# Kernel optimization log

Measured on AMD Instinct MI355X. Metric: run time of the kernel, lower is better.

The kernel has to match this reference:

```python
import jax, jax.numpy as jnp
import numpy as np

IN_C = 256
GROUPS = 32
ED = 256  # ResnetBlock embed_dim
EPS = 1e-5
B, L = 16, 2048


def setup_inputs() -> dict:
    key = jax.random.key(0)
    ks = jax.random.split(key, 8)

    def rn(k, shape, s=0.05):
        return jax.random.normal(k, shape, dtype=jnp.float32) * s

    d = {
        "x": jax.random.normal(ks[0], (B, IN_C, L), dtype=jnp.float32),
        "t": jax.random.normal(ks[1], (B, 256, 1), dtype=jnp.float32),
    }
    i = 2
    for p in ["r1", "r2"]:
        d[f"{p}_gn1_w"] = jnp.ones((IN_C,), jnp.float32)
        d[f"{p}_gn1_b"] = jnp.zeros((IN_C,), jnp.float32)
        d[f"{p}_c1_w"] = rn(ks[i], (ED, IN_C, 3)); i += 1
        d[f"{p}_c1_b"] = jnp.zeros((ED,), jnp.float32)
        d[f"{p}_gn2_w"] = jnp.ones((ED,), jnp.float32)
        d[f"{p}_gn2_b"] = jnp.zeros((ED,), jnp.float32)
        d[f"{p}_c2_w"] = rn(ks[i], (IN_C, ED, 3)); i += 1
        d[f"{p}_c2_b"] = jnp.zeros((IN_C,), jnp.float32)
    d["lin_w"] = rn(ks[i], (3 * IN_C, IN_C, 1))
    d["lin_b"] = jnp.zeros((3 * IN_C,), jnp.float32)
    return d


def _gn(x, w, b):
    # GroupNorm over (C//G, L) per group, affine per-channel
    Bx, C, Lx = x.shape
    xr = x.reshape(Bx, GROUPS, -1)
    m = xr.mean(-1, keepdims=True)
    v = xr.var(-1, keepdims=True)
    xr = (xr - m) * jax.lax.rsqrt(v + EPS)
    return xr.reshape(Bx, C, Lx) * w[None, :, None] + b[None, :, None]


def _conv(x, w, b, pad):
    y = jax.lax.conv_general_dilated(
        x, w, window_strides=(1,), padding=[(pad, pad)],
        dimension_numbers=("NCH", "OIH", "NCH"))
    return y + b[None, :, None]


def _res(x, t, gn1w, gn1b, c1w, c1b, gn2w, gn2b, c2w, c2b):
    h = _conv(jax.nn.relu(_gn(x, gn1w, gn1b)), c1w, c1b, 1) + t
    h = _conv(jax.nn.relu(_gn(h, gn2w, gn2b)), c2w, c2b, 1)
    return x + h


def reference(x, t,
              r1_gn1_w, r1_gn1_b, r1_c1_w, r1_c1_b, r1_gn2_w, r1_gn2_b, r1_c2_w, r1_c2_b,
              r2_gn1_w, r2_gn1_b, r2_c1_w, r2_c1_b, r2_gn2_w, r2_gn2_b, r2_c2_w, r2_c2_b,
              lin_w, lin_b):
    x = _res(x, t, r1_gn1_w, r1_gn1_b, r1_c1_w, r1_c1_b, r1_gn2_w, r1_gn2_b, r1_c2_w, r1_c2_b)
    kqv = _conv(x, lin_w, lin_b, 0)                      # (B, 3C, L)
    kt, qt, vt = jnp.split(kqv, 3, axis=1)               # each (B, C, L)
    scale = 1.0 / np.sqrt(x.shape[1]).astype(np.float32)
    scores = jnp.einsum("bcq,bck->bqk", qt, kt) * scale  # (B, L, L)
    attn = jax.nn.softmax(scores, axis=2)
    av = jnp.einsum("bqk,bck->bcq", attn, vt)            # (B, C, L)
    return _res(av, t, r2_gn1_w, r2_gn1_b, r2_c1_w, r2_c1_b, r2_gn2_w, r2_gn2_b, r2_c2_w, r2_c2_b)
```

## Files before the change

kernel.cpp:

```cpp
#include <hip/hip_runtime.h>

typedef unsigned short u16;
typedef unsigned int u32;
typedef __attribute__((ext_vector_type(8))) short bf16x8;
typedef __attribute__((ext_vector_type(4))) float f32x4;
typedef __attribute__((ext_vector_type(16))) float f32x16;

#define NB 16
#define NC 256
#define NL 2048
#define NG 32
#define EPS 1e-5f
#define QSC2 0.0901684401f
#define DEFER 11.54f
#define TROWS 2050
#define PHALF ((size_t)NB * NC * NL)

__device__ __forceinline__ float bf2f(u16 a) {
  union { unsigned u; float f; } v; v.u = (unsigned)a << 16; return v.f;
}
__device__ __forceinline__ u16 f2bf(float f) {
  union { float f; unsigned u; } v; v.f = f;
  return (u16)((v.u + 0x7fffu + ((v.u >> 16) & 1u)) >> 16);
}
__device__ __forceinline__ u32 cvtpk(float lo, float hi) {
  u32 r;
  asm("v_cvt_pk_bf16_f32 %0, %1, %2" : "=v"(r) : "v"(lo), "v"(hi));
  return r;
}
__device__ __forceinline__ float ex2(float x) {
  float r;
  asm("v_exp_f32 %0, %1" : "=v"(r) : "v"(x));
  return r;
}
__device__ __forceinline__ void gld16(const void* gsrc, void* ldst) {
  __builtin_amdgcn_global_load_lds(
      (const __attribute__((address_space(1))) void*)gsrc,
      (__attribute__((address_space(3))) void*)ldst, 16, 0, 0);
}

__global__ __launch_bounds__(256)
void pack_w(const float* __restrict__ w1, const float* __restrict__ w2,
            const float* __restrict__ w3, const float* __restrict__ w4,
            const float* __restrict__ lw, const float* __restrict__ lb,
            u16* __restrict__ Wp, u16* __restrict__ Wq, float* __restrict__ bq)
{
  const int a = blockIdx.y;
  const int gid = blockIdx.x * 256 + threadIdx.x;
  if (a < 4) {
    const float* w = a == 0 ? w1 : a == 1 ? w2 : a == 2 ? w3 : w4;
    const int d = gid >> 16, rem = gid & 65535;
    const int oc = rem >> 8, ic = rem & 255;
    Wp[a * 196608 + gid] = f2bf(w[(oc * 256 + ic) * 3 + d]);
  } else {
    const int oc = gid >> 8;
    const float s = (oc >= 256 && oc < 512) ? QSC2 : 1.0f;
    Wq[gid] = f2bf(lw[gid] * s);
    if (gid < 768) bq[gid] = lb[gid] * ((gid >= 256 && gid < 512) ? QSC2 : 1.0f);
  }
}

__global__ __launch_bounds__(256)
void stats_f32(const float* __restrict__ x, float2* __restrict__ pstat)
{
  const int blk = blockIdx.x;
  const float* p = x + (size_t)blk * NL + threadIdx.x * 8;
  const float4 a = ((const float4*)p)[0];
  const float4 c4 = ((const float4*)p)[1];
  float s = (a.x + a.y) + (a.z + a.w) + (c4.x + c4.y) + (c4.z + c4.w);
  float ss = a.x*a.x + a.y*a.y + a.z*a.z + a.w*a.w + c4.x*c4.x + c4.y*c4.y + c4.z*c4.z + c4.w*c4.w;
#pragma unroll
  for (int o = 32; o > 0; o >>= 1) { s += __shfl_down(s, o); ss += __shfl_down(ss, o); }
  __shared__ float2 red[4];
  if ((threadIdx.x & 63) == 0) red[threadIdx.x >> 6] = make_float2(s, ss);
  __syncthreads();
  if (threadIdx.x == 0)
    pstat[blk] = make_float2(red[0].x + red[1].x + red[2].x + red[3].x,
                             red[0].y + red[1].y + red[2].y + red[3].y);
}

__global__ __launch_bounds__(256)
void stats_T(const u16* __restrict__ inT, float2* __restrict__ pstat)
{
  const int chunk = blockIdx.x, b = blockIdx.y;
  const int t = threadIdx.x;
  const int c4 = (t & 63) * 4;
  float s[4] = {0.f, 0.f, 0.f, 0.f}, ss[4] = {0.f, 0.f, 0.f, 0.f};
  for (int j = 0; j < 32; ++j) {
    const int row = chunk * 128 + j * 4 + (t >> 6);
    const ushort4 h = *(const ushort4*)(inT + ((size_t)b * TROWS + 1 + row) * 256 + c4);
    const float v0 = bf2f(h.x), v1 = bf2f(h.y), v2 = bf2f(h.z), v3 = bf2f(h.w);
    s[0] += v0; ss[0] += v0 * v0;
    s[1] += v1; ss[1] += v1 * v1;
    s[2] += v2; ss[2] += v2 * v2;
    s[3] += v3; ss[3] += v3 * v3;
  }
  __shared__ float2 srs[256][4];
#pragma unroll
  for (int i = 0; i < 4; ++i) srs[t][i] = make_float2(s[i], ss[i]);
  __syncthreads();
  if (t < 64) {
#pragma unroll
    for (int r = 1; r < 4; ++r)
#pragma unroll
      for (int i = 0; i < 4; ++i) {
        s[i] += srs[t + 64 * r][i].x;
        ss[i] += srs[t + 64 * r][i].y;
      }
#pragma unroll
    for (int i = 0; i < 4; ++i)
      pstat[((size_t)b * 16 + chunk) * 256 + t * 4 + i] = make_float2(s[i], ss[i]);
  }
}

__global__ __launch_bounds__(256)
void apply_f32T(const float* __restrict__ x, const float2* __restrict__ pstat,
                const float* __restrict__ gw, const float* __restrict__ gb,
                u16* __restrict__ outT)
{
  __shared__ float2 chs[256];
  __shared__ float gm[32], gi[32];
  __shared__ float ta[256][33];
  const int t = threadIdx.x, b = blockIdx.y;
  const int L0 = blockIdx.x * 32;
  chs[t] = pstat[b * 256 + t];
  __syncthreads();
  if (t < 32) {
    float S = 0.f, SS = 0.f;
#pragma unroll
    for (int j = 0; j < 8; ++j) { S += chs[t * 8 + j].x; SS += chs[t * 8 + j].y; }
    const float mean = S * (1.f / 16384.f);
    const float var = SS * (1.f / 16384.f) - mean * mean;
    gm[t] = mean; gi[t] = rsqrtf(var + EPS);
  }
  const int cR = t >> 3, lq = (t & 7) * 4;
#pragma unroll
  for (int i = 0; i < 8; ++i) {
    const int c = i * 32 + cR;
    const float4 v = *(const float4*)&x[((size_t)b * NC + c) * NL + L0 + lq];
    ta[c][lq] = v.x; ta[c][lq + 1] = v.y; ta[c][lq + 2] = v.z; ta[c][lq + 3] = v.w;
  }
  __syncthreads();
  const int g = t & 31;
  float ga[8], be[8];
#pragma unroll
  for (int j = 0; j < 8; ++j) {
    ga[j] = gw[g * 8 + j] * gi[g];
    be[j] = gb[g * 8 + j] - gm[g] * ga[j];
  }
#pragma unroll
  for (int i = 0; i < 4; ++i) {
    const int chunk = i * 256 + t;
    const int row = chunk >> 5;
    const int ch8 = g * 8;
    u16 o[8];
#pragma unroll
    for (int j = 0; j < 8; ++j)
      o[j] = f2bf(fmaxf(fmaf(ta[ch8 + j][row], ga[j], be[j]), 0.f));
    *(bf16x8*)(outT + ((size_t)b * TROWS + 1 + L0 + row) * 256 + ch8) = *(bf16x8*)o;
  }
  if (blockIdx.x == 0 && t < 128) {
    const int r = (t >> 6) ? 2049 : 0;
    *(ushort4*)(outT + ((size_t)b * TROWS + r) * 256 + (t & 63) * 4) = (ushort4){0, 0, 0, 0};
  }
}

__global__ __launch_bounds__(256)
void apply_TT(const u16* __restrict__ inT, const float2* __restrict__ pstat,
              const float* __restrict__ gw, const float* __restrict__ gb,
              u16* __restrict__ outT)
{
  __shared__ float2 chs[256];
  __shared__ float gm[32], gi[32];
  const int t = threadIdx.x, b = blockIdx.y;
  {
    float S = 0.f, SS = 0.f;
#pragma unroll
    for (int p = 0; p < 16; ++p) {
      const float2 v = pstat[((size_t)b * 16 + p) * 256 + t];
      S += v.x; SS += v.y;
    }
    chs[t] = make_float2(S, SS);
  }
  __syncthreads();
  if (t < 32) {
    float S = 0.f, SS = 0.f;
#pragma unroll
    for (int j = 0; j < 8; ++j) { S += chs[t * 8 + j].x; SS += chs[t * 8 + j].y; }
    const float mean = S * (1.f / 16384.f);
    const float var = SS * (1.f / 16384.f) - mean * mean;
    gm[t] = mean; gi[t] = rsqrtf(var + EPS);
  }
  __syncthreads();
  const int g = t & 31;
  float ga[8], be[8];
#pragma unroll
  for (int j = 0; j < 8; ++j) {
    ga[j] = gw[g * 8 + j] * gi[g];
    be[j] = gb[g * 8 + j] - gm[g] * ga[j];
  }
#pragma unroll
  for (int j = 0; j < 16; ++j) {
    const int row = blockIdx.x * 128 + j * 8 + (t >> 5);
    const size_t off = ((size_t)b * TROWS + 1 + row) * 256 + g * 8;
    const bf16x8 h = *(const bf16x8*)(inT + off);
    u16 o[8];
#pragma unroll
    for (int i = 0; i < 8; ++i)
      o[i] = f2bf(fmaxf(fmaf(bf2f(((const u16*)&h)[i]), ga[i], be[i]), 0.f));
    *(bf16x8*)(outT + off) = *(bf16x8*)o;
  }
  if (blockIdx.x == 0 && t < 128) {
    const int r = (t >> 6) ? 2049 : 0;
    *(ushort4*)(outT + ((size_t)b * TROWS + r) * 256 + (t & 63) * 4) = (ushort4){0, 0, 0, 0};
  }
}

template<int OCT, int KD, bool HAS_T, int RESM>
__global__ __launch_bounds__(256, 2)
void conv_mfma(const u16* __restrict__ xT, const u16* __restrict__ Wp,
               const float* __restrict__ bias, const float* __restrict__ tadd,
               u16* __restrict__ outT, u16* __restrict__ vTout,
               const float* __restrict__ resf, float* __restrict__ outf)
{
  constexpr int DOFF = (KD == 3) ? 0 : 1;
  __shared__ __align__(16) u16 xs[2][130 * 128];
  const int lb = blockIdx.x * 128;
  const int ocb = blockIdx.y * 128;
  const int b = blockIdx.z;
  const int tid = threadIdx.x;
  const int w = tid >> 6, lane = tid & 63;
  const int l15 = lane & 15, lg = lane >> 4;
  const int woc = (w >> 1) * 64, wl = (w & 1) * 64;

  f32x4 acc[4][4];
#pragma unroll
  for (int i = 0; i < 4; ++i)
#pragma unroll
    for (int j = 0; j < 4; ++j) acc[i][j] = (f32x4){0.f, 0.f, 0.f, 0.f};

  const u16* xTb = xT + ((size_t)b * TROWS + lb) * 256;

  auto stageX = [&](int buf, int ich) {
    u16* xb = &xs[buf][0];
#pragma unroll
    for (int j = 0; j < 8; ++j) {
      const int slot = w * 512 + j * 64 + lane;
      const int row = slot >> 4, g0 = slot & 15;
      const int g = (g0 & 8) | ((g0 ^ row) & 7);
      gld16(xTb + (size_t)row * 256 + ich * 128 + g * 8, xb + (size_t)(w * 512 + j * 64) * 8);
    }
    if (w == 0 && lane < 32) {
      const int slot = 2048 + lane;
      const int row = slot >> 4, g0 = slot & 15;
      const int g = (g0 & 8) | ((g0 ^ row) & 7);
      gld16(xTb + (size_t)row * 256 + ich * 128 + g * 8, xb + (size_t)2048 * 8);
    }
  };
  auto loadW = [&](bf16x8 (&af)[KD][4], int p) {
    const int ich = p >> 2, kc = p & 3;
#pragma unroll
    for (int d = 0; d < KD; ++d)
#pragma unroll
      for (int mf = 0; mf < 4; ++mf)
        af[d][mf] = *(const bf16x8*)(Wp + ((size_t)d * OCT + ocb + woc + mf * 16 + l15) * 256
                                        + ich * 128 + kc * 32 + lg * 8);
  };

  bf16x8 afbuf[2][KD][4];
  stageX(0, 0);
  loadW(afbuf[0], 0);
  __syncthreads();
  stageX(1, 1);

#pragma unroll
  for (int p = 0; p < 8; ++p) {
    if (p == 4) __syncthreads();
    if (p < 7) loadW(afbuf[(p + 1) & 1], p + 1);
    const int kc = p & 3;
    const int gg = kc * 4 + lg;
    const char* xb = (const char*)&xs[p >> 2][0];
#pragma unroll
    for (int nf = 0; nf < 4; ++nf) {
#pragma unroll
      for (int d = 0; d < KD; ++d) {
        const int r = wl + nf * 16 + l15 + d + DOFF;
        const int gsr = (gg & 8) | ((gg ^ r) & 7);
        const bf16x8 bf = *(const bf16x8*)(xb + r * 256 + gsr * 16);
#pragma unroll
        for (int mf = 0; mf < 4; ++mf)
          acc[mf][nf] = __builtin_amdgcn_mfma_f32_16x16x32_bf16(afbuf[p & 1][d][mf], bf, acc[mf][nf], 0, 0, 0);
      }
    }
  }

  if (OCT == 768 && ocb >= 512) {
    __syncthreads();
    u16* tile = (u16*)&xs[0][0];
#pragma unroll
    for (int mf = 0; mf < 4; ++mf) {
      const int cl = woc + mf * 16 + lg * 4;
      const float4 bv = *(const float4*)&bias[ocb + cl];
#pragma unroll
      for (int nf = 0; nf < 4; ++nf) {
        const int ll = wl + nf * 16 + l15;
        const f32x4 a = acc[mf][nf];
        tile[(cl + 0) * 136 + ll] = f2bf(a[0] + bv.x);
        tile[(cl + 1) * 136 + ll] = f2bf(a[1] + bv.y);
        tile[(cl + 2) * 136 + ll] = f2bf(a[2] + bv.z);
        tile[(cl + 3) * 136 + ll] = f2bf(a[3] + bv.w);
      }
    }
    __syncthreads();
    const int cv0 = ocb - 512;
#pragma unroll
    for (int it = 0; it < 8; ++it) {
      const int chunk = it * 256 + tid;
      const int row = chunk >> 4, off = (chunk & 15) * 8;
      const bf16x8 v = *(const bf16x8*)&tile[row * 136 + off];
      *(bf16x8*)(vTout + ((size_t)b * NC + cv0 + row) * NL + lb + off) = v;
    }
    return;
  }

#pragma unroll
  for (int mf = 0; mf < 4; ++mf) {
    const int ocbase = ocb + woc + mf * 16 + lg * 4;
    float4 bv = *(const float4*)&bias[ocbase];
    if (HAS_T) {
      const float4 tv = *(const float4*)&tadd[b * 256 + ocbase];
      bv.x += tv.x; bv.y += tv.y; bv.z += tv.z; bv.w += tv.w;
    }
#pragma unroll
    for (int nf = 0; nf < 4; ++nf) {
      const int l = lb + wl + nf * 16 + l15;
      const f32x4 a = acc[mf][nf];
      float v0 = a[0] + bv.x, v1 = a[1] + bv.y, v2 = a[2] + bv.z, v3 = a[3] + bv.w;
      if (RESM >= 1) {
        const float* rp = resf + ((size_t)b * NC + ocbase) * NL + l;
        v0 += rp[0]; v1 += rp[NL]; v2 += rp[2 * (size_t)NL]; v3 += rp[3 * (size_t)NL];
      }
      if (RESM == 2) {
        float* op = outf + ((size_t)b * NC + ocbase) * NL + l;
        op[0] = v0; op[NL] = v1; op[2 * (size_t)NL] = v2; op[3 * (size_t)NL] = v3;
      } else if (OCT == 256) {
        ushort4 st = {f2bf(v0), f2bf(v1), f2bf(v2), f2bf(v3)};
        *(ushort4*)(outT + ((size_t)b * TROWS + 1 + l) * 256 + ocbase) = st;
      } else {
        ushort4 st = {f2bf(v0), f2bf(v1), f2bf(v2), f2bf(v3)};
        *(ushort4*)(outT + ((size_t)b * NL + l) * 512 + ocbase) = st;
      }
    }
  }
}

#define AKVB 32
#define ATILES 32

__global__ __launch_bounds__(256, 2)
void attn_mfma(const u16* __restrict__ kq, const u16* __restrict__ vT,
               u16* __restrict__ part, float2* __restrict__ stats)
{
  __shared__ u16 ks[2][32 * 256];
  __shared__ u16 vs[2][256 * 32];

  const int fid = blockIdx.x;
  const int xcd = fid & 7, idx = fid >> 3;
  const int b = (xcd << 1) | (idx & 1);
  const int rest = idx >> 1;
  const int qt = rest & 15, half = rest >> 4;
  const int kvbase = half * 1024;

  const int tid = threadIdx.x;
  const int w = tid >> 6, lane = tid & 63;
  const int l31 = lane & 31, lh = lane >> 5;
  const int q = qt * 128 + w * 32 + l31;

  const u16* kqb = kq + (size_t)b * NL * 512;
  const u16* vb  = vT + (size_t)b * NC * NL;

  auto stage = [&](int buf, int kv0) {
#pragma unroll
    for (int j = 0; j < 4; ++j) {
      const int slot = w * 256 + j * 64 + lane;
      const int r = slot >> 5, c = slot & 31;
      const int g = (c - r) & 31;
      gld16(kqb + (size_t)(kv0 + r) * 512 + g * 8, &ks[buf][(size_t)(w * 256 + j * 64) * 8]);
    }
#pragma unroll
    for (int j = 0; j < 4; ++j) {
      const int slot = w * 256 + j * 64 + lane;
      const int r = slot >> 2, c = slot & 3;
      const int g = (c - r - (r >> 2)) & 3;
      gld16(vb + (size_t)r * NL + kv0 + g * 8, &vs[buf][(size_t)(w * 256 + j * 64) * 8]);
    }
  };

  bf16x8 qf[16];
  {
    const u16* qp = kqb + (size_t)q * 512 + 256 + lh * 8;
#pragma unroll
    for (int kk = 0; kk < 16; ++kk) qf[kk] = *(const bf16x8*)(qp + kk * 16);
  }

  f32x16 o[8];
#pragma unroll
  for (int i = 0; i < 8; ++i)
    o[i] = (f32x16){0.f,0.f,0.f,0.f,0.f,0.f,0.f,0.f,0.f,0.f,0.f,0.f,0.f,0.f,0.f,0.f};
  float m = -1e30f, lsum = 0.f;

  stage(0, kvbase);
  __syncthreads();

  for (int t = 0; t < ATILES; ++t) {
    const int cur = t & 1;
    if (t + 1 < ATILES) stage(cur ^ 1, kvbase + (t + 1) * AKVB);
    const u16* kbase = &ks[cur][0];
    f32x16 s = (f32x16){0.f,0.f,0.f,0.f,0.f,0.f,0.f,0.f,0.f,0.f,0.f,0.f,0.f,0.f,0.f,0.f};
#pragma unroll
    for (int kk = 0; kk < 16; ++kk) {
      const int gn = 2 * kk + lh;
      const bf16x8 kf = *(const bf16x8*)(kbase + (l31 * 32 + ((gn + l31) & 31)) * 8);
      s = __builtin_amdgcn_mfma_f32_32x32x16_bf16(kf, qf[kk], s, 0, 0, 0);
    }
    float tm = s[0];
#pragma unroll
    for (int i = 1; i < 16; ++i) tm = fmaxf(tm, s[i]);
    tm = fmaxf(tm, __shfl_xor(tm, 32));
    if (!__all(tm <= m + DEFER)) {
      const float mn = fmaxf(m, tm);
      const float corr = ex2(m - mn);
      m = mn; lsum *= corr;
#pragma unroll
      for (int i = 0; i < 8; ++i) o[i] *= corr;
    }
    float sum = 0.f;
#pragma unroll
    for (int i = 0; i < 16; ++i) { s[i] = ex2(s[i] - m); sum += s[i]; }
    sum += __shfl_xor(sum, 32);
    lsum += sum;
    u32 pk[8];
#pragma unroll
    for (int i = 0; i < 8; ++i) pk[i] = cvtpk(s[2 * i], s[2 * i + 1]);
    const u16* vbase = &vs[cur][0];
#pragma unroll
    for (int ksx = 0; ksx < 2; ++ksx) {
      const int base = ksx * 4;
      const u32 send0 = lh ? pk[base + 0] : pk[base + 2];
      const u32 send1 = lh ? pk[base + 1] : pk[base + 3];
      const u32 r0 = (u32)__shfl_xor((int)send0, 32);
      const u32 r1 = (u32)__shfl_xor((int)send1, 32);
      union { u32 wd[4]; bf16x8 v; } pu;
      pu.wd[0] = lh ? r0 : pk[base + 0];
      pu.wd[1] = lh ? r1 : pk[base + 1];
      pu.wd[2] = lh ? pk[base + 2] : r0;
      pu.wd[3] = lh ? pk[base + 3] : r1;
      const bf16x8 pf = pu.v;
      const int gn = 2 * ksx + lh;
#pragma unroll
      for (int mf = 0; mf < 8; ++mf) {
        const int row = mf * 32 + l31;
        const bf16x8 vf = *(const bf16x8*)(vbase + (row * 4 + ((gn + row + (row >> 2)) & 3)) * 8);
        o[mf] = __builtin_amdgcn_mfma_f32_32x32x16_bf16(vf, pf, o[mf], 0, 0, 0);
      }
    }
    if (t + 1 < ATILES) __syncthreads();
  }
  u16* pp = part + half * PHALF + (size_t)b * NC * NL + q;
#pragma unroll
  for (int mf = 0; mf < 8; ++mf)
#pragma unroll
    for (int r = 0; r < 16; ++r) {
      const int c = mf * 32 + (r & 3) + 8 * (r >> 2) + 4 * lh;
      pp[(size_t)c * NL] = f2bf(o[mf][r]);
    }
  if (lane < 32)
    stats[((size_t)half * NB + b) * NL + q] = make_float2(m, lsum);
}

__global__ __launch_bounds__(256)
void attn_combine(const u16* __restrict__ part, const float2* __restrict__ stats,
                  float* __restrict__ av, float2* __restrict__ pstat)
{
  const int c = blockIdx.x, b = blockIdx.y;
  const u16* p0 = part + ((size_t)b * NC + c) * NL;
  const u16* p1 = p0 + PHALF;
  const float2* s0p = stats + (size_t)b * NL;
  const float2* s1p = stats + ((size_t)NB + b) * NL;
  float* op = av + ((size_t)b * NC + c) * NL;
  float s = 0.f, ss = 0.f;
#pragma unroll
  for (int j = 0; j < 8; ++j) {
    const int l = threadIdx.x + j * 256;
    const float2 a = s0p[l], bb = s1p[l];
    const float M = fmaxf(a.x, bb.x);
    const float e0 = ex2(a.x - M), e1 = ex2(bb.x - M);
    const float den = 1.f / (a.y * e0 + bb.y * e1);
    const float r = (bf2f(p0[l]) * e0 + bf2f(p1[l]) * e1) * den;
    op[l] = r;
    s += r; ss += r * r;
  }
#pragma unroll
  for (int o = 32; o > 0; o >>= 1) { s += __shfl_down(s, o); ss += __shfl_down(ss, o); }
  __shared__ float2 red[4];
  if ((threadIdx.x & 63) == 0) red[threadIdx.x >> 6] = make_float2(s, ss);
  __syncthreads();
  if (threadIdx.x == 0)
    pstat[b * 256 + c] = make_float2(red[0].x + red[1].x + red[2].x + red[3].x,
                                     red[0].y + red[1].y + red[2].y + red[3].y);
}

extern "C" void kernel_launch(void* const* d_in, const int* in_sizes, int n_in,
                              void* d_out, int out_size, void* d_ws, size_t ws_size,
                              hipStream_t stream)
{
  (void)in_sizes; (void)n_in; (void)out_size; (void)ws_size;
  const float* x        = (const float*)d_in[0];
  const float* t        = (const float*)d_in[1];
  const float* r1_gn1_w = (const float*)d_in[2];
  const float* r1_gn1_b = (const float*)d_in[3];
  const float* r1_c1_w  = (const float*)d_in[4];
  const float* r1_c1_b  = (const float*)d_in[5];
  const float* r1_gn2_w = (const float*)d_in[6];
  const float* r1_gn2_b = (const float*)d_in[7];
  const float* r1_c2_w  = (const float*)d_in[8];
  const float* r1_c2_b  = (const float*)d_in[9];
  const float* r2_gn1_w = (const float*)d_in[10];
  const float* r2_gn1_b = (const float*)d_in[11];
  const float* r2_c1_w  = (const float*)d_in[12];
  const float* r2_c1_b  = (const float*)d_in[13];
  const float* r2_gn2_w = (const float*)d_in[14];
  const float* r2_gn2_b = (const float*)d_in[15];
  const float* r2_c2_w  = (const float*)d_in[16];
  const float* r2_c2_b  = (const float*)d_in[17];
  const float* lin_w    = (const float*)d_in[18];
  const float* lin_b    = (const float*)d_in[19];

  float* out = (float*)d_out;

  const size_t TSZ = (size_t)NB * TROWS * 256 * 2;
  u16* tA  = (u16*)d_ws;
  u16* tB  = (u16*)((char*)d_ws + TSZ);
  u16* kq  = tB;
  float* avF = (float*)((char*)d_ws + TSZ);
  u16* tC  = (u16*)((char*)d_ws + 3 * TSZ);
  u16* vT  = tC;
  u16* Wp  = (u16*)((char*)d_ws + 4 * TSZ);
  u16* Wq  = Wp + 4 * 196608;
  float* bq = (float*)(Wq + 196608);
  float2* pstat = (float2*)((char*)bq + 4096);

  const dim3 gPack(768, 5);
  const dim3 gC(16, 2, NB);
  const dim3 gQ(16, 6, NB);
  const dim3 gS16(16, NB);
  const dim3 gA64(64, NB);
  const dim3 gCmb(NC, NB);

  pack_w<<<gPack, 256, 0, stream>>>(r1_c1_w, r1_c2_w, r2_c1_w, r2_c2_w, lin_w, lin_b, Wp, Wq, bq);

  stats_f32<<<NB * NC, 256, 0, stream>>>(x, pstat);
  apply_f32T<<<gA64, 256, 0, stream>>>(x, pstat, r1_gn1_w, r1_gn1_b, tA);
  conv_mfma<256, 3, true, 0><<<gC, 256, 0, stream>>>(tA, Wp, r1_c1_b, t, tB, nullptr, nullptr, nullptr);
  stats_T<<<gS16, 256, 0, stream>>>(tB, pstat);
  apply_TT<<<gS16, 256, 0, stream>>>(tB, pstat, r1_gn2_w, r1_gn2_b, tC);
  conv_mfma<256, 3, false, 1><<<gC, 256, 0, stream>>>(tC, Wp + 196608, r1_c2_b, nullptr, tA, nullptr, x, nullptr);

  conv_mfma<768, 1, false, 0><<<gQ, 256, 0, stream>>>(tA, Wq, bq, nullptr, kq, vT, nullptr, nullptr);
  attn_mfma<<<512, 256, 0, stream>>>(kq, vT, (u16*)out, (float2*)tA);
  attn_combine<<<gCmb, 256, 0, stream>>>((const u16*)out, (const float2*)tA, avF, pstat);

  apply_f32T<<<gA64, 256, 0, stream>>>(avF, pstat, r2_gn1_w, r2_gn1_b, tA);
  conv_mfma<256, 3, true, 0><<<gC, 256, 0, stream>>>(tA, Wp + 2 * 196608, r2_c1_b, t, tC, nullptr, nullptr, nullptr);
  stats_T<<<gS16, 256, 0, stream>>>(tC, pstat);
  apply_TT<<<gS16, 256, 0, stream>>>(tC, pstat, r2_gn2_w, r2_gn2_b, tA);
  conv_mfma<256, 3, false, 2><<<gC, 256, 0, stream>>>(tA, Wp + 3 * 196608, r2_c2_b, nullptr, nullptr, nullptr, avF, out);
}
```

Measured before the change: 368.1 us.

## Process two query tiles per attention wave, vectorize combine and transpose apply

The attention kernel now has each wave handle 64 queries (two 32-query MFMA tiles), so every K and V fragment read from LDS feeds two MFMAs. The grid is halved to 256 blocks and occupancy drops to one block per CU to fit the doubled register state. The combine kernel now reads 8 contiguous elements per thread with vector loads and stores. The GroupNorm apply kernel's LDS transpose is re-laid out to change its access pattern. The risks are register pressure with fewer waves to hide latency, and only 256 blocks to fill the GPU.

```diff
diff --git a/kernel.cpp b/kernel.cpp
--- a/kernel.cpp
+++ b/kernel.cpp
@@ -9,7 +9,6 @@
 #define NB 16
 #define NC 256
 #define NL 2048
-#define NG 32
 #define EPS 1e-5f
 #define QSC2 0.0901684401f
 #define DEFER 11.54f
@@ -120,7 +119,7 @@
 {
   __shared__ float2 chs[256];
   __shared__ float gm[32], gi[32];
-  __shared__ float ta[256][33];
+  __shared__ float ta[32][257];
   const int t = threadIdx.x, b = blockIdx.y;
   const int L0 = blockIdx.x * 32;
   chs[t] = pstat[b * 256 + t];
@@ -133,31 +132,40 @@
     const float var = SS * (1.f / 16384.f) - mean * mean;
     gm[t] = mean; gi[t] = rsqrtf(var + EPS);
   }
-  const int cR = t >> 3, lq = (t & 7) * 4;
-#pragma unroll
-  for (int i = 0; i < 8; ++i) {
-    const int c = i * 32 + cR;
-    const float4 v = *(const float4*)&x[((size_t)b * NC + c) * NL + L0 + lq];
-    ta[c][lq] = v.x; ta[c][lq + 1] = v.y; ta[c][lq + 2] = v.z; ta[c][lq + 3] = v.w;
-  }
-  __syncthreads();
-  const int g = t & 31;
+  {
+    const int cR = t >> 3, lq = (t & 7) * 4;
+#pragma unroll
+    for (int i = 0; i < 8; ++i) {
+      const int c = i * 32 + cR;
+      const float4 v = *(const float4*)&x[((size_t)b * NC + c) * NL + L0 + lq];
+      ta[lq + 0][c] = v.x; ta[lq + 1][c] = v.y; ta[lq + 2][c] = v.z; ta[lq + 3][c] = v.w;
+    }
+  }
+  __syncthreads();
+  const int g = t & 31, rbase = t >> 5;
   float ga[8], be[8];
 #pragma unroll
-  for (int j = 0; j < 8; ++j) {
-    ga[j] = gw[g * 8 + j] * gi[g];
-    be[j] = gb[g * 8 + j] - gm[g] * ga[j];
-  }
-#pragma unroll
-  for (int i = 0; i < 4; ++i) {
-    const int chunk = i * 256 + t;
-    const int row = chunk >> 5;
-    const int ch8 = g * 8;
-    u16 o[8];
-#pragma unroll
-    for (int j = 0; j < 8; ++j)
-      o[j] = f2bf(fmaxf(fmaf(ta[ch8 + j][row], ga[j], be[j]), 0.f));
-    *(bf16x8*)(outT + ((size_t)b * TROWS + 1 + L0 + row) * 256 + ch8) = *(bf16x8*)o;
+  for (int j = 0; j < 4; ++j)
+#pragma unroll
+    for (int k = 0; k < 2; ++k) {
+      const int c = 2 * g + 64 * j + k;
+      const int grp = c >> 3;
+      ga[j * 2 + k] = gw[c] * gi[grp];
+      be[j * 2 + k] = gb[c] - gm[grp] * ga[j * 2 + k];
+    }
+#pragma unroll
+  for (int ri = 0; ri < 4; ++ri) {
+    const int row = rbase + ri * 8;
+    u16* orow = outT + ((size_t)b * TROWS + 1 + L0 + row) * 256;
+#pragma unroll
+    for (int j = 0; j < 4; ++j) {
+      const int c = 2 * g + 64 * j;
+      const float v0 = ta[row][c], v1 = ta[row][c + 1];
+      ushort2 o;
+      o.x = f2bf(fmaxf(fmaf(v0, ga[j * 2], be[j * 2]), 0.f));
+      o.y = f2bf(fmaxf(fmaf(v1, ga[j * 2 + 1], be[j * 2 + 1]), 0.f));
+      *(ushort2*)(orow + c) = o;
+    }
   }
   if (blockIdx.x == 0 && t < 128) {
     const int r = (t >> 6) ? 2049 : 0;
@@ -357,7 +365,7 @@
 #define AKVB 32
 #define ATILES 32
 
-__global__ __launch_bounds__(256, 2)
+__global__ __launch_bounds__(256, 1)
 void attn_mfma(const u16* __restrict__ kq, const u16* __restrict__ vT,
                u16* __restrict__ part, float2* __restrict__ stats)
 {
@@ -368,13 +376,13 @@
   const int xcd = fid & 7, idx = fid >> 3;
   const int b = (xcd << 1) | (idx & 1);
   const int rest = idx >> 1;
-  const int qt = rest & 15, half = rest >> 4;
+  const int qt = rest & 7, half = rest >> 3;
   const int kvbase = half * 1024;
 
   const int tid = threadIdx.x;
   const int w = tid >> 6, lane = tid & 63;
   const int l31 = lane & 31, lh = lane >> 5;
-  const int q = qt * 128 + w * 32 + l31;
+  const int qb = qt * 256 + w * 64;
 
   const u16* kqb = kq + (size_t)b * NL * 512;
   const u16* vb  = vT + (size_t)b * NC * NL;
@@ -396,18 +404,24 @@
     }
   };
 
-  bf16x8 qf[16];
+  bf16x8 qfA[16], qfB[16];
   {
-    const u16* qp = kqb + (size_t)q * 512 + 256 + lh * 8;
-#pragma unroll
-    for (int kk = 0; kk < 16; ++kk) qf[kk] = *(const bf16x8*)(qp + kk * 16);
-  }
-
-  f32x16 o[8];
-#pragma unroll
-  for (int i = 0; i < 8; ++i)
-    o[i] = (f32x16){0.f,0.f,0.f,0.f,0.f,0.f,0.f,0.f,0.f,0.f,0.f,0.f,0.f,0.f,0.f,0.f};
-  float m = -1e30f, lsum = 0.f;
+    const u16* qpA = kqb + (size_t)(qb + l31) * 512 + 256 + lh * 8;
+    const u16* qpB = qpA + 32 * 512;
+#pragma unroll
+    for (int kk = 0; kk < 16; ++kk) {
+      qfA[kk] = *(const bf16x8*)(qpA + kk * 16);
+      qfB[kk] = *(const bf16x8*)(qpB + kk * 16);
+    }
+  }
+
+  f32x16 oA[8], oB[8];
+#pragma unroll
+  for (int i = 0; i < 8; ++i) {
+    oA[i] = (f32x16){0.f,0.f,0.f,0.f,0.f,0.f,0.f,0.f,0.f,0.f,0.f,0.f,0.f,0.f,0.f,0.f};
+    oB[i] = oA[i];
+  }
+  float mA = -1e30f, lsA = 0.f, mB = -1e30f, lsB = 0.f;
 
   stage(0, kvbase);
   __syncthreads();
@@ -416,66 +430,97 @@
     const int cur = t & 1;
     if (t + 1 < ATILES) stage(cur ^ 1, kvbase + (t + 1) * AKVB);
     const u16* kbase = &ks[cur][0];
-    f32x16 s = (f32x16){0.f,0.f,0.f,0.f,0.f,0.f,0.f,0.f,0.f,0.f,0.f,0.f,0.f,0.f,0.f,0.f};
+    f32x16 sA = (f32x16){0.f,0.f,0.f,0.f,0.f,0.f,0.f,0.f,0.f,0.f,0.f,0.f,0.f,0.f,0.f,0.f};
+    f32x16 sB = sA;
 #pragma unroll
     for (int kk = 0; kk < 16; ++kk) {
       const int gn = 2 * kk + lh;
       const bf16x8 kf = *(const bf16x8*)(kbase + (l31 * 32 + ((gn + l31) & 31)) * 8);
-      s = __builtin_amdgcn_mfma_f32_32x32x16_bf16(kf, qf[kk], s, 0, 0, 0);
-    }
-    float tm = s[0];
-#pragma unroll
-    for (int i = 1; i < 16; ++i) tm = fmaxf(tm, s[i]);
+      sA = __builtin_amdgcn_mfma_f32_32x32x16_bf16(kf, qfA[kk], sA, 0, 0, 0);
+      sB = __builtin_amdgcn_mfma_f32_32x32x16_bf16(kf, qfB[kk], sB, 0, 0, 0);
+    }
+    float tm = sA[0];
+#pragma unroll
+    for (int i = 1; i < 16; ++i) tm = fmaxf(tm, sA[i]);
     tm = fmaxf(tm, __shfl_xor(tm, 32));
-    if (!__all(tm <= m + DEFER)) {
-      const float mn = fmaxf(m, tm);
-      const float corr = ex2(m - mn);
-      m = mn; lsum *= corr;
-#pragma unroll
-      for (int i = 0; i < 8; ++i) o[i] *= corr;
+    if (!__all(tm <= mA + DEFER)) {
+      const float mn = fmaxf(mA, tm);
+      const float corr = ex2(mA - mn);
+      mA = mn; lsA *= corr;
+#pragma unroll
+      for (int i = 0; i < 8; ++i) oA[i] *= corr;
     }
     float sum = 0.f;
 #pragma unroll
-    for (int i = 0; i < 16; ++i) { s[i] = ex2(s[i] - m); sum += s[i]; }
+    for (int i = 0; i < 16; ++i) { sA[i] = ex2(sA[i] - mA); sum += sA[i]; }
     sum += __shfl_xor(sum, 32);
-    lsum += sum;
-    u32 pk[8];
-#pragma unroll
-    for (int i = 0; i < 8; ++i) pk[i] = cvtpk(s[2 * i], s[2 * i + 1]);
+    lsA += sum;
+    tm = sB[0];
+#pragma unroll
+    for (int i = 1; i < 16; ++i) tm = fmaxf(tm, sB[i]);
+    tm = fmaxf(tm, __shfl_xor(tm, 32));
+    if (!__all(tm <= mB + DEFER)) {
+      const float mn = fmaxf(mB, tm);
+      const float corr = ex2(mB - mn);
+      mB = mn; lsB *= corr;
+#pragma unroll
+      for (int i = 0; i < 8; ++i) oB[i] *= corr;
+    }
+    sum = 0.f;
+#pragma unroll
+    for (int i = 0; i < 16; ++i) { sB[i] = ex2(sB[i] - mB); sum += sB[i]; }
+    sum += __shfl_xor(sum, 32);
+    lsB += sum;
+    u32 pkA[8], pkB[8];
+#pragma unroll
+    for (int i = 0; i < 8; ++i) {
+      pkA[i] = cvtpk(sA[2 * i], sA[2 * i + 1]);
+      pkB[i] = cvtpk(sB[2 * i], sB[2 * i + 1]);
+    }
     const u16* vbase = &vs[cur][0];
 #pragma unroll
     for (int ksx = 0; ksx < 2; ++ksx) {
       const int base = ksx * 4;
-      const u32 send0 = lh ? pk[base + 0] : pk[base + 2];
-      const u32 send1 = lh ? pk[base + 1] : pk[base + 3];
-      const u32 r0 = (u32)__shfl_xor((int)send0, 32);
-      const u32 r1 = (u32)__shfl_xor((int)send1, 32);
-      union { u32 wd[4]; bf16x8 v; } pu;
-      pu.wd[0] = lh ? r0 : pk[base + 0];
-      pu.wd[1] = lh ? r1 : pk[base + 1];
-      pu.wd[2] = lh ? pk[base + 2] : r0;
-      pu.wd[3] = lh ? pk[base + 3] : r1;
-      const bf16x8 pf = pu.v;
+      const u32 sA0 = lh ? pkA[base + 0] : pkA[base + 2];
+      const u32 sA1 = lh ? pkA[base + 1] : pkA[base + 3];
+      const u32 sB0 = lh ? pkB[base + 0] : pkB[base + 2];
+      const u32 sB1 = lh ? pkB[base + 1] : pkB[base + 3];
+      const u32 rA0 = (u32)__shfl_xor((int)sA0, 32);
+      const u32 rA1 = (u32)__shfl_xor((int)sA1, 32);
+      const u32 rB0 = (u32)__shfl_xor((int)sB0, 32);
+      const u32 rB1 = (u32)__shfl_xor((int)sB1, 32);
+      union { u32 wd[4]; bf16x8 v; } puA, puB;
+      puA.wd[0] = lh ? rA0 : pkA[base + 0];
+      puA.wd[1] = lh ? rA1 : pkA[base + 1];
+      puA.wd[2] = lh ? pkA[base + 2] : rA0;
+      puA.wd[3] = lh ? pkA[base + 3] : rA1;
+      puB.wd[0] = lh ? rB0 : pkB[base + 0];
+      puB.wd[1] = lh ? rB1 : pkB[base + 1];
+      puB.wd[2] = lh ? pkB[base + 2] : rB0;
+      puB.wd[3] = lh ? pkB[base + 3] : rB1;
+      const bf16x8 pfA = puA.v, pfB = puB.v;
       const int gn = 2 * ksx + lh;
 #pragma unroll
       for (int mf = 0; mf < 8; ++mf) {
         const int row = mf * 32 + l31;
         const bf16x8 vf = *(const bf16x8*)(vbase + (row * 4 + ((gn + row + (row >> 2)) & 3)) * 8);
-        o[mf] = __builtin_amdgcn_mfma_f32_32x32x16_bf16(vf, pf, o[mf], 0, 0, 0);
+        oA[mf] = __builtin_amdgcn_mfma_f32_32x32x16_bf16(vf, pfA, oA[mf], 0, 0, 0);
+        oB[mf] = __builtin_amdgcn_mfma_f32_32x32x16_bf16(vf, pfB, oB[mf], 0, 0, 0);
       }
     }
     if (t + 1 < ATILES) __syncthreads();
   }
-  u16* pp = part + half * PHALF + (size_t)b * NC * NL + q;
+  u16* pp = part + half * PHALF + (size_t)b * NC * NL + qb + l31;
 #pragma unroll
   for (int mf = 0; mf < 8; ++mf)
 #pragma unroll
     for (int r = 0; r < 16; ++r) {
       const int c = mf * 32 + (r & 3) + 8 * (r >> 2) + 4 * lh;
-      pp[(size_t)c * NL] = f2bf(o[mf][r]);
-    }
-  if (lane < 32)
-    stats[((size_t)half * NB + b) * NL + q] = make_float2(m, lsum);
+      pp[(size_t)c * NL] = f2bf(oA[mf][r]);
+      pp[(size_t)c * NL + 32] = f2bf(oB[mf][r]);
+    }
+  stats[((size_t)half * NB + b) * NL + qb + lane] =
+      (lane < 32) ? make_float2(mA, lsA) : make_float2(mB, lsB);
 }
 
 __global__ __launch_bounds__(256)
@@ -483,23 +528,28 @@
                   float* __restrict__ av, float2* __restrict__ pstat)
 {
   const int c = blockIdx.x, b = blockIdx.y;
-  const u16* p0 = part + ((size_t)b * NC + c) * NL;
+  const int l0 = threadIdx.x * 8;
+  const u16* p0 = part + ((size_t)b * NC + c) * NL + l0;
   const u16* p1 = p0 + PHALF;
-  const float2* s0p = stats + (size_t)b * NL;
-  const float2* s1p = stats + ((size_t)NB + b) * NL;
-  float* op = av + ((size_t)b * NC + c) * NL;
+  const float2* s0p = stats + (size_t)b * NL + l0;
+  const float2* s1p = stats + ((size_t)NB + b) * NL + l0;
+  const bf16x8 P0 = *(const bf16x8*)p0;
+  const bf16x8 P1 = *(const bf16x8*)p1;
+  float* op = av + ((size_t)b * NC + c) * NL + l0;
   float s = 0.f, ss = 0.f;
+  float res[8];
 #pragma unroll
   for (int j = 0; j < 8; ++j) {
-    const int l = threadIdx.x + j * 256;
-    const float2 a = s0p[l], bb = s1p[l];
+    const float2 a = s0p[j], bb = s1p[j];
     const float M = fmaxf(a.x, bb.x);
     const float e0 = ex2(a.x - M), e1 = ex2(bb.x - M);
     const float den = 1.f / (a.y * e0 + bb.y * e1);
-    const float r = (bf2f(p0[l]) * e0 + bf2f(p1[l]) * e1) * den;
-    op[l] = r;
+    const float r = (bf2f(((const u16*)&P0)[j]) * e0 + bf2f(((const u16*)&P1)[j]) * e1) * den;
+    res[j] = r;
     s += r; ss += r * r;
   }
+  *(float4*)op = make_float4(res[0], res[1], res[2], res[3]);
+  *(float4*)(op + 4) = make_float4(res[4], res[5], res[6], res[7]);
 #pragma unroll
   for (int o = 32; o > 0; o >>= 1) { s += __shfl_down(s, o); ss += __shfl_down(ss, o); }
   __shared__ float2 red[4];
@@ -567,7 +617,7 @@
   conv_mfma<256, 3, false, 1><<<gC, 256, 0, stream>>>(tC, Wp + 196608, r1_c2_b, nullptr, tA, nullptr, x, nullptr);
 
   conv_mfma<768, 1, false, 0><<<gQ, 256, 0, stream>>>(tA, Wq, bq, nullptr, kq, vT, nullptr, nullptr);
-  attn_mfma<<<512, 256, 0, stream>>>(kq, vT, (u16*)out, (float2*)tA);
+  attn_mfma<<<256, 256, 0, stream>>>(kq, vT, (u16*)out, (float2*)tA);
   attn_combine<<<gCmb, 256, 0, stream>>>((const u16*)out, (const float2*)tA, avF, pstat);
 
   apply_f32T<<<gA64, 256, 0, stream>>>(avF, pstat, r2_gn1_w, r2_gn1_b, tA);
```

Result: slower. 864.3 us (+134.8%).

## Fuse GroupNorm stats into conv epilogue, retile apply and vectorize combine

Applied to the files above, without the earlier changes.

Removes the separate stats_T kernels by accumulating per-channel sum and sum-of-squares in the conv_mfma epilogue, then reducing across lanes and waves through shared memory into pstat. It also changes the apply_f32T shared transpose layout to avoid bank conflicts and writes smaller chunks. attn_combine now uses vectorized bf16x8 loads and float4 stores. Stats are taken from fp32 values before bf16 rounding, so the numbers differ slightly, and the conv epilogue gains extra registers and a barrier.

```diff
diff --git a/kernel.cpp b/kernel.cpp
--- a/kernel.cpp
+++ b/kernel.cpp
@@ -9,7 +9,6 @@
 #define NB 16
 #define NC 256
 #define NL 2048
-#define NG 32
 #define EPS 1e-5f
 #define QSC2 0.0901684401f
 #define DEFER 11.54f
@@ -80,47 +79,13 @@
 }
 
 __global__ __launch_bounds__(256)
-void stats_T(const u16* __restrict__ inT, float2* __restrict__ pstat)
-{
-  const int chunk = blockIdx.x, b = blockIdx.y;
-  const int t = threadIdx.x;
-  const int c4 = (t & 63) * 4;
-  float s[4] = {0.f, 0.f, 0.f, 0.f}, ss[4] = {0.f, 0.f, 0.f, 0.f};
-  for (int j = 0; j < 32; ++j) {
-    const int row = chunk * 128 + j * 4 + (t >> 6);
-    const ushort4 h = *(const ushort4*)(inT + ((size_t)b * TROWS + 1 + row) * 256 + c4);
-    const float v0 = bf2f(h.x), v1 = bf2f(h.y), v2 = bf2f(h.z), v3 = bf2f(h.w);
-    s[0] += v0; ss[0] += v0 * v0;
-    s[1] += v1; ss[1] += v1 * v1;
-    s[2] += v2; ss[2] += v2 * v2;
-    s[3] += v3; ss[3] += v3 * v3;
-  }
-  __shared__ float2 srs[256][4];
-#pragma unroll
-  for (int i = 0; i < 4; ++i) srs[t][i] = make_float2(s[i], ss[i]);
-  __syncthreads();
-  if (t < 64) {
-#pragma unroll
-    for (int r = 1; r < 4; ++r)
-#pragma unroll
-      for (int i = 0; i < 4; ++i) {
-        s[i] += srs[t + 64 * r][i].x;
-        ss[i] += srs[t + 64 * r][i].y;
-      }
-#pragma unroll
-    for (int i = 0; i < 4; ++i)
-      pstat[((size_t)b * 16 + chunk) * 256 + t * 4 + i] = make_float2(s[i], ss[i]);
-  }
-}
-
-__global__ __launch_bounds__(256)
 void apply_f32T(const float* __restrict__ x, const float2* __restrict__ pstat,
                 const float* __restrict__ gw, const float* __restrict__ gb,
                 u16* __restrict__ outT)
 {
   __shared__ float2 chs[256];
   __shared__ float gm[32], gi[32];
-  __shared__ float ta[256][33];
+  __shared__ float ta[32][257];
   const int t = threadIdx.x, b = blockIdx.y;
   const int L0 = blockIdx.x * 32;
   chs[t] = pstat[b * 256 + t];
@@ -133,31 +98,40 @@
     const float var = SS * (1.f / 16384.f) - mean * mean;
     gm[t] = mean; gi[t] = rsqrtf(var + EPS);
   }
-  const int cR = t >> 3, lq = (t & 7) * 4;
-#pragma unroll
-  for (int i = 0; i < 8; ++i) {
-    const int c = i * 32 + cR;
-    const float4 v = *(const float4*)&x[((size_t)b * NC + c) * NL + L0 + lq];
-    ta[c][lq] = v.x; ta[c][lq + 1] = v.y; ta[c][lq + 2] = v.z; ta[c][lq + 3] = v.w;
-  }
-  __syncthreads();
-  const int g = t & 31;
+  {
+    const int cR = t >> 3, lq = (t & 7) * 4;
+#pragma unroll
+    for (int i = 0; i < 8; ++i) {
+      const int c = i * 32 + cR;
+      const float4 v = *(const float4*)&x[((size_t)b * NC + c) * NL + L0 + lq];
+      ta[lq + 0][c] = v.x; ta[lq + 1][c] = v.y; ta[lq + 2][c] = v.z; ta[lq + 3][c] = v.w;
+    }
+  }
+  __syncthreads();
+  const int g = t & 31, rbase = t >> 5;
   float ga[8], be[8];
 #pragma unroll
-  for (int j = 0; j < 8; ++j) {
-    ga[j] = gw[g * 8 + j] * gi[g];
-    be[j] = gb[g * 8 + j] - gm[g] * ga[j];
-  }
-#pragma unroll
-  for (int i = 0; i < 4; ++i) {
-    const int chunk = i * 256 + t;
-    const int row = chunk >> 5;
-    const int ch8 = g * 8;
-    u16 o[8];
-#pragma unroll
-    for (int j = 0; j < 8; ++j)
-      o[j] = f2bf(fmaxf(fmaf(ta[ch8 + j][row], ga[j], be[j]), 0.f));
-    *(bf16x8*)(outT + ((size_t)b * TROWS + 1 + L0 + row) * 256 + ch8) = *(bf16x8*)o;
+  for (int j = 0; j < 4; ++j)
+#pragma unroll
+    for (int k = 0; k < 2; ++k) {
+      const int c = 2 * g + 64 * j + k;
+      const int grp = c >> 3;
+      ga[j * 2 + k] = gw[c] * gi[grp];
+      be[j * 2 + k] = gb[c] - gm[grp] * ga[j * 2 + k];
+    }
+#pragma unroll
+  for (int ri = 0; ri < 4; ++ri) {
+    const int row = rbase + ri * 8;
+    u16* orow = outT + ((size_t)b * TROWS + 1 + L0 + row) * 256;
+#pragma unroll
+    for (int j = 0; j < 4; ++j) {
+      const int c = 2 * g + 64 * j;
+      const float v0 = ta[row][c], v1 = ta[row][c + 1];
+      ushort2 o;
+      o.x = f2bf(fmaxf(fmaf(v0, ga[j * 2], be[j * 2]), 0.f));
+      o.y = f2bf(fmaxf(fmaf(v1, ga[j * 2 + 1], be[j * 2 + 1]), 0.f));
+      *(ushort2*)(orow + c) = o;
+    }
   }
   if (blockIdx.x == 0 && t < 128) {
     const int r = (t >> 6) ? 2049 : 0;
@@ -216,12 +190,13 @@
   }
 }
 
-template<int OCT, int KD, bool HAS_T, int RESM>
+template<int OCT, int KD, bool HAS_T, int RESM, bool STATS>
 __global__ __launch_bounds__(256, 2)
 void conv_mfma(const u16* __restrict__ xT, const u16* __restrict__ Wp,
                const float* __restrict__ bias, const float* __restrict__ tadd,
                u16* __restrict__ outT, u16* __restrict__ vTout,
-               const float* __restrict__ resf, float* __restrict__ outf)
+               const float* __restrict__ resf, float* __restrict__ outf,
+               float2* __restrict__ pstatOut)
 {
   constexpr int DOFF = (KD == 3) ? 0 : 1;
   __shared__ __align__(16) u16 xs[2][130 * 128];
@@ -323,6 +298,14 @@
     return;
   }
 
+  float cs[4][4], cq[4][4];
+  if (STATS) {
+#pragma unroll
+    for (int i = 0; i < 4; ++i)
+#pragma unroll
+      for (int j = 0; j < 4; ++j) { cs[i][j] = 0.f; cq[i][j] = 0.f; }
+  }
+
 #pragma unroll
   for (int mf = 0; mf < 4; ++mf) {
     const int ocbase = ocb + woc + mf * 16 + lg * 4;
@@ -339,6 +322,12 @@
       if (RESM >= 1) {
         const float* rp = resf + ((size_t)b * NC + ocbase) * NL + l;
         v0 += rp[0]; v1 += rp[NL]; v2 += rp[2 * (size_t)NL]; v3 += rp[3 * (size_t)NL];
+      }
+      if (STATS) {
+        cs[mf][0] += v0; cq[mf][0] += v0 * v0;
+        cs[mf][1] += v1; cq[mf][1] += v1 * v1;
+        cs[mf][2] += v2; cq[mf][2] += v2 * v2;
+        cs[mf][3] += v3; cq[mf][3] += v3 * v3;
       }
       if (RESM == 2) {
         float* op = outf + ((size_t)b * NC + ocbase) * NL + l;
@@ -350,6 +339,30 @@
         ushort4 st = {f2bf(v0), f2bf(v1), f2bf(v2), f2bf(v3)};
         *(ushort4*)(outT + ((size_t)b * NL + l) * 512 + ocbase) = st;
       }
+    }
+  }
+
+  if (STATS) {
+    __syncthreads();
+    float* sred = (float*)&xs[0][0];
+#pragma unroll
+    for (int mf = 0; mf < 4; ++mf)
+#pragma unroll
+      for (int j = 0; j < 4; ++j) {
+        float s = cs[mf][j], q = cq[mf][j];
+#pragma unroll
+        for (int m = 1; m < 16; m <<= 1) { s += __shfl_xor(s, m); q += __shfl_xor(q, m); }
+        if (l15 == 0) {
+          const int cl = woc + mf * 16 + lg * 4 + j;
+          sred[(w & 1) * 128 + cl] = s;
+          sred[256 + (w & 1) * 128 + cl] = q;
+        }
+      }
+    __syncthreads();
+    if (tid < 128) {
+      const float s = sred[tid] + sred[128 + tid];
+      const float q = sred[256 + tid] + sred[384 + tid];
+      pstatOut[((size_t)b * 16 + blockIdx.x) * 256 + ocb + tid] = make_float2(s, q);
     }
   }
 }
@@ -483,23 +496,28 @@
                   float* __restrict__ av, float2* __restrict__ pstat)
 {
   const int c = blockIdx.x, b = blockIdx.y;
-  const u16* p0 = part + ((size_t)b * NC + c) * NL;
+  const int l0 = threadIdx.x * 8;
+  const u16* p0 = part + ((size_t)b * NC + c) * NL + l0;
   const u16* p1 = p0 + PHALF;
-  const float2* s0p = stats + (size_t)b * NL;
-  const float2* s1p = stats + ((size_t)NB + b) * NL;
-  float* op = av + ((size_t)b * NC + c) * NL;
+  const float2* s0p = stats + (size_t)b * NL + l0;
+  const float2* s1p = stats + ((size_t)NB + b) * NL + l0;
+  const bf16x8 P0 = *(const bf16x8*)p0;
+  const bf16x8 P1 = *(const bf16x8*)p1;
+  float* op = av + ((size_t)b * NC + c) * NL + l0;
   float s = 0.f, ss = 0.f;
+  float res[8];
 #pragma unroll
   for (int j = 0; j < 8; ++j) {
-    const int l = threadIdx.x + j * 256;
-    const float2 a = s0p[l], bb = s1p[l];
+    const float2 a = s0p[j], bb = s1p[j];
     const float M = fmaxf(a.x, bb.x);
     const float e0 = ex2(a.x - M), e1 = ex2(bb.x - M);
     const float den = 1.f / (a.y * e0 + bb.y * e1);
-    const float r = (bf2f(p0[l]) * e0 + bf2f(p1[l]) * e1) * den;
-    op[l] = r;
+    const float r = (bf2f(((const u16*)&P0)[j]) * e0 + bf2f(((const u16*)&P1)[j]) * e1) * den;
+    res[j] = r;
     s += r; ss += r * r;
   }
+  *(float4*)op = make_float4(res[0], res[1], res[2], res[3]);
+  *(float4*)(op + 4) = make_float4(res[4], res[5], res[6], res[7]);
 #pragma unroll
   for (int o = 32; o > 0; o >>= 1) { s += __shfl_down(s, o); ss += __shfl_down(ss, o); }
   __shared__ float2 red[4];
@@ -561,18 +579,16 @@
 
   stats_f32<<<NB * NC, 256, 0, stream>>>(x, pstat);
   apply_f32T<<<gA64, 256, 0, stream>>>(x, pstat, r1_gn1_w, r1_gn1_b, tA);
-  conv_mfma<256, 3, true, 0><<<gC, 256, 0, stream>>>(tA, Wp, r1_c1_b, t, tB, nullptr, nullptr, nullptr);
-  stats_T<<<gS16, 256, 0, stream>>>(tB, pstat);
+  conv_mfma<256, 3, true, 0, true><<<gC, 256, 0, stream>>>(tA, Wp, r1_c1_b, t, tB, nullptr, nullptr, nullptr, pstat);
   apply_TT<<<gS16, 256, 0, stream>>>(tB, pstat, r1_gn2_w, r1_gn2_b, tC);
-  conv_mfma<256, 3, false, 1><<<gC, 256, 0, stream>>>(tC, Wp + 196608, r1_c2_b, nullptr, tA, nullptr, x, nullptr);
-
-  conv_mfma<768, 1, false, 0><<<gQ, 256, 0, stream>>>(tA, Wq, bq, nullptr, kq, vT, nullptr, nullptr);
+  conv_mfma<256, 3, false, 1, false><<<gC, 256, 0, stream>>>(tC, Wp + 196608, r1_c2_b, nullptr, tA, nullptr, x, nullptr, nullptr);
+
+  conv_mfma<768, 1, false, 0, false><<<gQ, 256, 0, stream>>>(tA, Wq, bq, nullptr, kq, vT, nullptr, nullptr, nullptr);
   attn_mfma<<<512, 256, 0, stream>>>(kq, vT, (u16*)out, (float2*)tA);
   attn_combine<<<gCmb, 256, 0, stream>>>((const u16*)out, (const float2*)tA, avF, pstat);
 
   apply_f32T<<<gA64, 256, 0, stream>>>(avF, pstat, r2_gn1_w, r2_gn1_b, tA);
-  conv_mfma<256, 3, true, 0><<<gC, 256, 0, stream>>>(tA, Wp + 2 * 196608, r2_c1_b, t, tC, nullptr, nullptr, nullptr);
-  stats_T<<<gS16, 256, 0, stream>>>(tC, pstat);
+  conv_mfma<256, 3, true, 0, true><<<gC, 256, 0, stream>>>(tA, Wp + 2 * 196608, r2_c1_b, t, tC, nullptr, nullptr, nullptr, pstat);
   apply_TT<<<gS16, 256, 0, stream>>>(tC, pstat, r2_gn2_w, r2_gn2_b, tA);
-  conv_mfma<256, 3, false, 2><<<gC, 256, 0, stream>>>(tA, Wp + 3 * 196608, r2_c2_b, nullptr, nullptr, nullptr, avF, out);
-}
+  conv_mfma<256, 3, false, 2, false><<<gC, 256, 0, stream>>>(tA, Wp + 3 * 196608, r2_c2_b, nullptr, nullptr, nullptr, avF, out, nullptr);
+}
```

After: 357.2 us. 1.03x faster.
